# Performance work log

Hardware: AMD Instinct MI355X
Metric: run time of the kernel (lower is better)

## Reference

```python
import jax, jax.numpy as jnp
import numpy as np

H = 512  # hidden_size


def setup_inputs() -> dict:
    key = jax.random.key(0)
    ks = jax.random.split(key, 13)
    B, S, E, V = 64, 2048, 512, 32000
    s = 0.05
    return {
        "word_input": jax.random.randint(ks[0], (B,), 0, V),
        "last_hidden": jax.random.normal(ks[1], (1, B, H), jnp.float32),
        "encoder_outputs": jax.random.normal(ks[2], (S, B, H), jnp.float32),
        "emb": jax.random.normal(ks[3], (V, E), jnp.float32) * s,
        "attn_W": jax.random.normal(ks[4], (H, 2 * H), jnp.float32) * s,
        "attn_b": jax.random.normal(ks[5], (H,), jnp.float32) * s,
        "v": jax.random.normal(ks[6], (H,), jnp.float32) * s,
        "W_ih": jax.random.normal(ks[7], (3 * H, H + E), jnp.float32) * s,
        "W_hh": jax.random.normal(ks[8], (3 * H, H), jnp.float32) * s,
        "b_ih": jax.random.normal(ks[9], (3 * H,), jnp.float32) * s,
        "b_hh": jax.random.normal(ks[10], (3 * H,), jnp.float32) * s,
        "out_W": jax.random.normal(ks[11], (V, 2 * H), jnp.float32) * s,
        "out_b": jax.random.normal(ks[12], (V,), jnp.float32) * s,
    }


def reference(word_input, last_hidden, encoder_outputs, emb, attn_W, attn_b, v,
              W_ih, W_hh, b_ih, b_hh, out_W, out_b):
    # word_input: [B] int; last_hidden: [1,B,H]; encoder_outputs: [S,B,H]
    hid = last_hidden[-1]                       # [B,H]
    enc = jnp.transpose(encoder_outputs, (1, 0, 2))  # [B,S,H]

    # Bahdanau 'concat' attention: tanh(W [h;e] + b) . v  (split W to avoid [B,S,2H])
    Wa, We = attn_W[:, :H], attn_W[:, H:]
    energy = jnp.tanh((hid @ Wa.T)[:, None, :] + jnp.einsum('bsh,kh->bsk', enc, We) + attn_b)
    scores = jnp.einsum('bsk,k->bs', energy, v)       # [B,S]
    attn = jax.nn.softmax(scores, axis=1)             # [B,S]
    context = jnp.einsum('bs,bsh->bh', attn, enc)     # [B,H]

    # GRU step (PyTorch gate layout: r, z, n)
    x = jnp.concatenate([emb[word_input], context], axis=1)  # [B,E+H]
    gi = x @ W_ih.T + b_ih
    gh = hid @ W_hh.T + b_hh
    r = jax.nn.sigmoid(gi[:, :H] + gh[:, :H])
    z = jax.nn.sigmoid(gi[:, H:2 * H] + gh[:, H:2 * H])
    n = jnp.tanh(gi[:, 2 * H:] + r * gh[:, 2 * H:])
    h_new = (1.0 - z) * n + z * hid                   # [B,H]

    logits = jnp.concatenate([h_new, context], axis=1) @ out_W.T + out_b
    output = jax.nn.log_softmax(logits, axis=1)       # [B,V]
    return output, h_new[None]                        # hidden: [1,B,H]
```

## Files before the change

kernel.cpp:

```cpp
#include <hip/hip_runtime.h>
#include <hip/hip_bf16.h>
#include <cstdint>
#include <cstddef>

#define HD 512
#define BB 64
#define SS 2048
#define VV 32000
#define MM (SS*BB)
#define NCH 32

typedef __attribute__((ext_vector_type(8))) short bf16x8;
typedef __attribute__((ext_vector_type(4))) float f32x4;

static __device__ __forceinline__ unsigned pack2(float a, float b) {
    unsigned r;
    asm("v_cvt_pk_bf16_f32 %0, %1, %2" : "=v"(r) : "v"(a), "v"(b));
    return r;
}
static __device__ __forceinline__ float rcp_fast(float x) {
    float r; asm("v_rcp_f32 %0, %1" : "=v"(r) : "v"(x)); return r;
}
static __device__ __forceinline__ float tanh_fast(float x) {
    float e = __expf(2.f * x);
    return 1.f - 2.f * rcp_fast(e + 1.f);
}
static __device__ __forceinline__ float sigmoid_fast(float x) {
    return 1.f / (1.f + __expf(-x));
}
static __device__ __forceinline__ void gload16(const void* g, void* l) {
    __builtin_amdgcn_global_load_lds(
        (const __attribute__((address_space(1))) void*)g,
        (__attribute__((address_space(3))) void*)l, 16, 0, 0);
}

#define WAITL   asm volatile("s_waitcnt lgkmcnt(0)" ::: "memory")
#define WAITVL(N) asm volatile("s_waitcnt vmcnt(" #N ") lgkmcnt(0)" ::: "memory")
#define SBAR    __builtin_amdgcn_s_barrier()
#define SCHED   __builtin_amdgcn_sched_barrier(0)

__global__ void prep_kernel(const float* __restrict__ hid,
                            const float* __restrict__ attn_W,
                            const float* __restrict__ attn_b,
                            float* __restrict__ qc,
                            uint4* __restrict__ WeB4) {
    int i = blockIdx.x * 256 + threadIdx.x;
    int n = i >> 6, b = i & 63;
    const float* hrow = hid + b * HD;
    const float* wrow = attn_W + (size_t)n * (2 * HD);
    float acc = 0.f;
    for (int k = 0; k < HD; k += 4) {
        float4 h4 = *(const float4*)(hrow + k);
        float4 w4 = *(const float4*)(wrow + k);
        acc += h4.x * w4.x + h4.y * w4.y + h4.z * w4.z + h4.w * w4.w;
    }
    qc[b * HD + n] = acc + attn_b[n];
    int col = (i << 3) & 511;
    int cc0 = col >> 3;
    const float* src = attn_W + (size_t)n * (2 * HD) + HD + col;
    float4 f0 = *(const float4*)(src);
    float4 f1 = *(const float4*)(src + 4);
    uint4 p;
    p.x = pack2(f0.x, f0.y); p.y = pack2(f0.z, f0.w);
    p.z = pack2(f1.x, f1.y); p.w = pack2(f1.z, f1.w);
    WeB4[n * 64 + cc0] = p;
}

__global__ __launch_bounds__(512, 4) void fattn_kernel(
    const float* __restrict__ enc,
    const uint4* __restrict__ WeB4,
    const float* __restrict__ qc,
    const float* __restrict__ vvec,
    float* __restrict__ oP,
    float* __restrict__ lP)
{
    __shared__ uint4 Ald[64 * 8];
    __shared__ float red[64][8];
    __shared__ float p_lds[64];
    __shared__ float opart[8 * 512];

    const int tid = threadIdx.x;
    const int wv = tid >> 6, lane = tid & 63, l15 = lane & 15, l4 = lane >> 4;
    const int b = blockIdx.x & 63;
    const int c = blockIdx.x >> 6;
    const int s0 = c * 64;

    f32x4 acc[4][4] = {};

    const int arow = tid >> 3;
    const int ac8 = tid & 7;
    const float* aptr = enc + ((size_t)(s0 + arow) * 64 + b) * HD + ac8 * 8;
    const int aslot = arow * 8 + (ac8 ^ (arow & 7));

    const uint4* bbase = WeB4 + (size_t)(wv * 64 + l15) * 64 + l4;

    float4 pa[2][2];
    pa[0][0] = *(const float4*)(aptr);
    pa[0][1] = *(const float4*)(aptr + 4);

#pragma unroll
    for (int t = 0; t < 8; ++t) {
        const int cur = t & 1;
        if (t > 0) { WAITL; SBAR; SCHED; }
        {
            uint4 u;
            u.x = pack2(pa[cur][0].x, pa[cur][0].y);
            u.y = pack2(pa[cur][0].z, pa[cur][0].w);
            u.z = pack2(pa[cur][1].x, pa[cur][1].y);
            u.w = pack2(pa[cur][1].z, pa[cur][1].w);
            Ald[aslot] = u;
        }
        if (t < 7) {
            pa[cur ^ 1][0] = *(const float4*)(aptr + (t + 1) * 64);
            pa[cur ^ 1][1] = *(const float4*)(aptr + (t + 1) * 64 + 4);
        }
        WAITL; SBAR; SCHED;

#pragma unroll
        for (int ks = 0; ks < 2; ++ks) {
            const int chunk = ks * 4 + l4;
            bf16x8 af[4], bfr[4];
#pragma unroll
            for (int mi = 0; mi < 4; ++mi) {
                int row = mi * 16 + l15;
                af[mi] = *(const bf16x8*)&Ald[row * 8 + (chunk ^ (row & 7))];
            }
#pragma unroll
            for (int ni = 0; ni < 4; ++ni)
                bfr[ni] = *(const bf16x8*)(bbase + ni * 16 * 64 + t * 8 + ks * 4);
#pragma unroll
            for (int mi = 0; mi < 4; ++mi)
#pragma unroll
                for (int ni = 0; ni < 4; ++ni)
                    acc[mi][ni] = __builtin_amdgcn_mfma_f32_16x16x32_bf16(
                        af[mi], bfr[ni], acc[mi][ni], 0, 0, 0);
        }
    }

    float vv[4], qn[4];
#pragma unroll
    for (int ni = 0; ni < 4; ++ni) {
        int n = wv * 64 + ni * 16 + l15;
        vv[ni] = vvec[n];
        qn[ni] = qc[b * HD + n];
    }
#pragma unroll
    for (int mi = 0; mi < 4; ++mi) {
#pragma unroll
        for (int r = 0; r < 4; ++r) {
            const int rowl = mi * 16 + l4 * 4 + r;
            float s = 0.f;
#pragma unroll
            for (int ni = 0; ni < 4; ++ni)
                s += tanh_fast(acc[mi][ni][r] + qn[ni]) * vv[ni];
#pragma unroll
            for (int msk = 8; msk >= 1; msk >>= 1)
                s += __shfl_xor(s, msk);
            if (l15 == 0) red[rowl][wv] = s;
        }
    }
    __syncthreads();
    if (tid < 64) {
        float t = ((red[tid][0] + red[tid][1]) + (red[tid][2] + red[tid][3]))
                + ((red[tid][4] + red[tid][5]) + (red[tid][6] + red[tid][7]));
        float p = __expf(t);
        p_lds[tid] = p;
        float l = p;
#pragma unroll
        for (int msk = 32; msk >= 1; msk >>= 1) l += __shfl_xor(l, msk);
        if (tid == 0) lP[b * NCH + c] = l;
    }
    __syncthreads();

    float o8[8] = {};
    const float* ebase = enc + ((size_t)(s0 + wv * 8) * 64 + b) * HD + lane * 8;
#pragma unroll
    for (int i = 0; i < 8; ++i) {
        float w = p_lds[wv * 8 + i];
        const float* ep = ebase + (size_t)i * 64 * HD;
        float4 e0 = *(const float4*)(ep);
        float4 e1 = *(const float4*)(ep + 4);
        o8[0] += w * e0.x; o8[1] += w * e0.y; o8[2] += w * e0.z; o8[3] += w * e0.w;
        o8[4] += w * e1.x; o8[5] += w * e1.y; o8[6] += w * e1.z; o8[7] += w * e1.w;
    }
    {
        float4* dst = (float4*)&opart[wv * 512 + lane * 8];
        float4 w0 = {o8[0], o8[1], o8[2], o8[3]};
        float4 w1 = {o8[4], o8[5], o8[6], o8[7]};
        dst[0] = w0; dst[1] = w1;
    }
    __syncthreads();
    float o = 0.f;
#pragma unroll
    for (int w = 0; w < 8; ++w) o += opart[w * 512 + tid];
    oP[((size_t)b * NCH + c) * HD + tid] = o;
}

__global__ void combine_kernel(const float* __restrict__ oP,
                               const float* __restrict__ lP,
                               const int* __restrict__ word,
                               const float* __restrict__ emb,
                               float* __restrict__ x,
                               unsigned* __restrict__ y_bf) {
    const int b = blockIdx.x;
    const int tid = threadIdx.x;
    __shared__ float ctx_lds[512];
    float L = 0.f;
#pragma unroll 8
    for (int c = 0; c < NCH; ++c) L += lP[b * NCH + c];
    float o = 0.f;
#pragma unroll 4
    for (int c = 0; c < NCH; ++c)
        o += oP[((size_t)b * NCH + c) * HD + tid];
    float ctx = o / L;
    x[b * 1024 + HD + tid] = ctx;
    ctx_lds[tid] = ctx;
    x[b * 1024 + tid] = emb[(size_t)word[b] * HD + tid];
    __syncthreads();
    if (tid < 256)
        y_bf[b * 512 + 256 + tid] = pack2(ctx_lds[2 * tid], ctx_lds[2 * tid + 1]);
}

__global__ void gates_kernel(const float* __restrict__ x,
                             const float* __restrict__ hid,
                             const float* __restrict__ W_ih,
                             const float* __restrict__ W_hh,
                             const float* __restrict__ b_ih,
                             const float* __restrict__ b_hh,
                             float* __restrict__ gi, float* __restrict__ gh) {
    const int tid = threadIdx.x;
    const int b = tid & 63;
    const int j = blockIdx.x * 4 + (tid >> 6);
    float agi = 0.f, agh = 0.f;
    const float* xr = x + b * 1024;
    const float* wr = W_ih + (size_t)j * 1024;
    for (int k = 0; k < 1024; k += 4) {
        float4 xv = *(const float4*)(xr + k);
        float4 w4 = *(const float4*)(wr + k);
        agi += xv.x * w4.x + xv.y * w4.y + xv.z * w4.z + xv.w * w4.w;
    }
    const float* hr = hid + b * HD;
    const float* wh = W_hh + (size_t)j * HD;
    for (int k = 0; k < HD; k += 4) {
        float4 hv = *(const float4*)(hr + k);
        float4 w4 = *(const float4*)(wh + k);
        agh += hv.x * w4.x + hv.y * w4.y + hv.z * w4.z + hv.w * w4.w;
    }
    gi[b * 1536 + j] = agi + b_ih[j];
    gh[b * 1536 + j] = agh + b_hh[j];
}

__global__ void hnew_kernel(const float* __restrict__ gi,
                            const float* __restrict__ gh,
                            const float* __restrict__ hid,
                            float* __restrict__ out_h,
                            unsigned* __restrict__ y_bf) {
    const int b = blockIdx.x;
    const int h = threadIdx.x * 2;
    float hn[2];
#pragma unroll
    for (int j = 0; j < 2; ++j) {
        int hh = h + j;
        float r = sigmoid_fast(gi[b * 1536 + hh] + gh[b * 1536 + hh]);
        float z = sigmoid_fast(gi[b * 1536 + 512 + hh] + gh[b * 1536 + 512 + hh]);
        float n = tanh_fast(gi[b * 1536 + 1024 + hh] + r * gh[b * 1536 + 1024 + hh]);
        hn[j] = (1.f - z) * n + z * hid[b * HD + hh];
        out_h[b * HD + hh] = hn[j];
    }
    y_bf[b * 512 + (h >> 1)] = pack2(hn[0], hn[1]);
}

__global__ __launch_bounds__(256, 4) void logits_kernel(
    const unsigned short* __restrict__ y_bf,
    const float* __restrict__ out_W,
    const float* __restrict__ out_b,
    float* __restrict__ logits)
{
    __shared__ uint4 Yld[64 * 8];
    __shared__ uint4 Wld[64 * 8];
    const int tid = threadIdx.x;
    const int wv = tid >> 6, lane = tid & 63, l15 = lane & 15, l4 = lane >> 4;
    const int n0 = blockIdx.x * 64;

    f32x4 acc[4] = {};

    const int s1 = tid, s2 = tid + 256;
    const int r1 = s1 >> 3, g1 = (s1 & 7) ^ (r1 & 7);
    const int r2 = s2 >> 3, g2 = (s2 & 7) ^ (r2 & 7);
    const unsigned short* ya1 = y_bf + (size_t)r1 * 1024 + g1 * 8;
    const unsigned short* ya2 = y_bf + (size_t)r2 * 1024 + g2 * 8;

    const int wr = tid >> 3, wc8 = tid & 7;
    const int wsl = wc8 ^ (wr & 7);
    const float* wp0 = out_W + (size_t)(n0 + wr) * 1024 + wc8 * 8;
    const float* wp1 = out_W + (size_t)(n0 + wr + 32) * 1024 + wc8 * 8;

    float4 pw[2][4];
    pw[0][0] = *(const float4*)(wp0);
    pw[0][1] = *(const float4*)(wp0 + 4);
    pw[0][2] = *(const float4*)(wp1);
    pw[0][3] = *(const float4*)(wp1 + 4);

#pragma unroll
    for (int t = 0; t < 16; ++t) {
        const int cur = t & 1;
        if (t > 0) {
            WAITL; SBAR; SCHED;
        }
        gload16(ya1 + t * 64, &Yld[s1]);
        gload16(ya2 + t * 64, &Yld[s2]);
        {
            uint4 u;
            u.x = pack2(pw[cur][0].x, pw[cur][0].y);
            u.y = pack2(pw[cur][0].z, pw[cur][0].w);
            u.z = pack2(pw[cur][1].x, pw[cur][1].y);
            u.w = pack2(pw[cur][1].z, pw[cur][1].w);
            Wld[wr * 8 + wsl] = u;
            u.x = pack2(pw[cur][2].x, pw[cur][2].y);
            u.y = pack2(pw[cur][2].z, pw[cur][2].w);
            u.z = pack2(pw[cur][3].x, pw[cur][3].y);
            u.w = pack2(pw[cur][3].z, pw[cur][3].w);
            Wld[(wr + 32) * 8 + wsl] = u;
        }
        if (t < 15) {
            const int k1 = (t + 1) * 64;
            pw[cur ^ 1][0] = *(const float4*)(wp0 + k1);
            pw[cur ^ 1][1] = *(const float4*)(wp0 + k1 + 4);
            pw[cur ^ 1][2] = *(const float4*)(wp1 + k1);
            pw[cur ^ 1][3] = *(const float4*)(wp1 + k1 + 4);
            WAITVL(4);
        } else {
            WAITVL(0);
        }
        SBAR; SCHED;

#pragma unroll
        for (int ks = 0; ks < 2; ++ks) {
            const int chunk = ks * 4 + l4;
            bf16x8 af[4], bfr;
#pragma unroll
            for (int mi = 0; mi < 4; ++mi) {
                int row = mi * 16 + l15;
                af[mi] = *(const bf16x8*)&Yld[row * 8 + (chunk ^ (row & 7))];
            }
            {
                int row = wv * 16 + l15;
                bfr = *(const bf16x8*)&Wld[row * 8 + (chunk ^ (row & 7))];
            }
#pragma unroll
            for (int mi = 0; mi < 4; ++mi)
                acc[mi] = __builtin_amdgcn_mfma_f32_16x16x32_bf16(
                    af[mi], bfr, acc[mi], 0, 0, 0);
        }
    }
#pragma unroll
    for (int mi = 0; mi < 4; ++mi) {
#pragma unroll
        for (int r = 0; r < 4; ++r) {
            const int b = mi * 16 + l4 * 4 + r;
            int n = n0 + wv * 16 + l15;
            logits[(size_t)b * VV + n] = acc[mi][r] + out_b[n];
        }
    }
}

__global__ void lsm1_kernel(const float* __restrict__ logits,
                            float* __restrict__ part) {
    const int bid = blockIdx.x;
    const int b = bid / 5, q = bid - b * 5;
    const int tid = threadIdx.x;
    __shared__ float sm[256];
    const float* row = logits + (size_t)b * VV + q * 6400;
    float m = -1e30f;
    for (int i = tid; i < 6400; i += 256) m = fmaxf(m, row[i]);
    sm[tid] = m; __syncthreads();
    for (int o = 128; o > 0; o >>= 1) {
        if (tid < o) sm[tid] = fmaxf(sm[tid], sm[tid + o]);
        __syncthreads();
    }
    m = sm[0]; __syncthreads();
    float s = 0.f;
    for (int i = tid; i < 6400; i += 256) s += __expf(row[i] - m);
    sm[tid] = s; __syncthreads();
    for (int o = 128; o > 0; o >>= 1) {
        if (tid < o) sm[tid] += sm[tid + o];
        __syncthreads();
    }
    if (tid == 0) { part[bid * 2] = m; part[bid * 2 + 1] = sm[0]; }
}

__global__ void lsm2_kernel(float* __restrict__ logits,
                            const float* __restrict__ part) {
    const int bid = blockIdx.x;
    const int b = bid / 5, q = bid - b * 5;
    const int tid = threadIdx.x;
    float m = -1e30f;
#pragma unroll
    for (int c = 0; c < 5; ++c) m = fmaxf(m, part[(b * 5 + c) * 2]);
    float L = 0.f;
#pragma unroll
    for (int c = 0; c < 5; ++c)
        L += part[(b * 5 + c) * 2 + 1] * __expf(part[(b * 5 + c) * 2] - m);
    float lse = m + __logf(L);
    float* row = logits + (size_t)b * VV + q * 6400;
    for (int i = tid; i < 6400; i += 256) row[i] -= lse;
}

extern "C" void kernel_launch(void* const* d_in, const int* in_sizes, int n_in,
                              void* d_out, int out_size, void* d_ws, size_t ws_size,
                              hipStream_t stream) {
    (void)in_sizes; (void)n_in; (void)out_size; (void)ws_size;
    const int*   word   = (const int*)d_in[0];
    const float* hid    = (const float*)d_in[1];
    const float* enc    = (const float*)d_in[2];
    const float* emb    = (const float*)d_in[3];
    const float* attn_W = (const float*)d_in[4];
    const float* attn_b = (const float*)d_in[5];
    const float* v      = (const float*)d_in[6];
    const float* W_ih   = (const float*)d_in[7];
    const float* W_hh   = (const float*)d_in[8];
    const float* b_ih   = (const float*)d_in[9];
    const float* b_hh   = (const float*)d_in[10];
    const float* out_W  = (const float*)d_in[11];
    const float* out_b  = (const float*)d_in[12];

    float* out    = (float*)d_out;
    float* logits = out;
    float* out_h  = out + (size_t)BB * VV;

    char* ws0 = (char*)d_ws;
    size_t off = 0;
    float* qc      = (float*)(ws0 + off);    off += 64 * 512 * 4;
    uint4* WeB4    = (uint4*)(ws0 + off);    off += 512 * 512 * 2;
    float* oP      = (float*)(ws0 + off);    off += (size_t)BB * NCH * HD * 4;
    float* lP      = (float*)(ws0 + off);    off += BB * NCH * 4;
    float* x       = (float*)(ws0 + off);    off += 64 * 1024 * 4;
    unsigned* y_bf = (unsigned*)(ws0 + off); off += 64 * 1024 * 2;
    float* gi      = (float*)(ws0 + off);    off += 64 * 1536 * 4;
    float* gh      = (float*)(ws0 + off);    off += 64 * 1536 * 4;
    float* lsmp    = (float*)(ws0 + off);    off += 320 * 2 * 4;

    prep_kernel<<<128, 256, 0, stream>>>(hid, attn_W, attn_b, qc, WeB4);
    fattn_kernel<<<BB * NCH, 512, 0, stream>>>(enc, WeB4, qc, v, oP, lP);
    combine_kernel<<<BB, 512, 0, stream>>>(oP, lP, word, emb, x, y_bf);
    gates_kernel<<<384, 256, 0, stream>>>(x, hid, W_ih, W_hh, b_ih, b_hh, gi, gh);
    hnew_kernel<<<BB, 256, 0, stream>>>(gi, gh, hid, out_h, y_bf);
    logits_kernel<<<VV / 64, 256, 0, stream>>>((const unsigned short*)y_bf, out_W, out_b, logits);
    lsm1_kernel<<<320, 256, 0, stream>>>(logits, lsmp);
    lsm2_kernel<<<320, 256, 0, stream>>>(logits, lsmp);
}
```

Before: 373.0 us.

## Stage full encoder tile in LDS upfront and pre-swizzle We into fragment order

The attention kernel now loads and converts the whole 64x512 encoder tile into a 64KB LDS buffer in one pass with a single barrier, replacing the per-k-step double-buffered register pipeline with its two barriers per step. The prep kernel writes the bf16 We matrix in MFMA-fragment order so each lane's B loads are contiguous and coalesced. opart aliases the same LDS. The larger LDS footprint (~66KB per 512-thread block) may lower occupancy below the launch-bounds target of 4 blocks, and global loads no longer overlap with MFMA work.

New measurement: 321.6 us. 13.8% less time.

```diff
diff --git a/kernel.cpp b/kernel.cpp
--- a/kernel.cpp
+++ b/kernel.cpp
@@ -43,9 +43,11 @@
                             const float* __restrict__ attn_W,
                             const float* __restrict__ attn_b,
                             float* __restrict__ qc,
-                            uint4* __restrict__ WeB4) {
+                            uint4* __restrict__ WeF) {
     int i = blockIdx.x * 256 + threadIdx.x;
-    int n = i >> 6, b = i & 63;
+    int n = i >> 6;
+    int cc = i & 63;
+    int b = i & 63;
     const float* hrow = hid + b * HD;
     const float* wrow = attn_W + (size_t)n * (2 * HD);
     float acc = 0.f;
@@ -55,29 +57,31 @@
         acc += h4.x * w4.x + h4.y * w4.y + h4.z * w4.z + h4.w * w4.w;
     }
     qc[b * HD + n] = acc + attn_b[n];
-    int col = (i << 3) & 511;
-    int cc0 = col >> 3;
-    const float* src = attn_W + (size_t)n * (2 * HD) + HD + col;
+    const float* src = attn_W + (size_t)n * (2 * HD) + HD + cc * 8;
     float4 f0 = *(const float4*)(src);
     float4 f1 = *(const float4*)(src + 4);
     uint4 p;
     p.x = pack2(f0.x, f0.y); p.y = pack2(f0.z, f0.w);
     p.z = pack2(f1.x, f1.y); p.w = pack2(f1.z, f1.w);
-    WeB4[n * 64 + cc0] = p;
+    int wv = n >> 6, ni = (n >> 4) & 3, l15 = n & 15;
+    int t = cc >> 3, ks = (cc >> 2) & 1, l4 = cc & 3;
+    int lane = l4 * 16 + l15;
+    WeF[((((wv * 8 + t) * 2 + ks) * 4 + ni) << 6) + lane] = p;
 }
 
 __global__ __launch_bounds__(512, 4) void fattn_kernel(
     const float* __restrict__ enc,
-    const uint4* __restrict__ WeB4,
+    const uint4* __restrict__ WeF,
     const float* __restrict__ qc,
     const float* __restrict__ vvec,
     float* __restrict__ oP,
     float* __restrict__ lP)
 {
-    __shared__ uint4 Ald[64 * 8];
-    __shared__ float red[64][8];
-    __shared__ float p_lds[64];
-    __shared__ float opart[8 * 512];
+    __shared__ char smem[65536 + 2048 + 256];
+    uint4* Ald = (uint4*)smem;
+    float (*red)[8] = (float(*)[8])(smem + 65536);
+    float* p_lds = (float*)(smem + 65536 + 2048);
+    float* opart = (float*)smem;
 
     const int tid = threadIdx.x;
     const int wv = tid >> 6, lane = tid & 63, l15 = lane & 15, l4 = lane >> 4;
@@ -85,49 +89,39 @@
     const int c = blockIdx.x >> 6;
     const int s0 = c * 64;
 
+    {
+        const int arow = tid >> 3, a8 = tid & 7;
+        const float* ap = enc + ((size_t)(s0 + arow) * 64 + b) * HD;
+#pragma unroll
+        for (int j = 0; j < 8; ++j) {
+            int cc = j * 8 + a8;
+            float4 f0 = *(const float4*)(ap + cc * 8);
+            float4 f1 = *(const float4*)(ap + cc * 8 + 4);
+            uint4 u;
+            u.x = pack2(f0.x, f0.y); u.y = pack2(f0.z, f0.w);
+            u.z = pack2(f1.x, f1.y); u.w = pack2(f1.z, f1.w);
+            Ald[arow * 64 + j * 8 + (a8 ^ (arow & 7))] = u;
+        }
+    }
+    __syncthreads();
+
     f32x4 acc[4][4] = {};
-
-    const int arow = tid >> 3;
-    const int ac8 = tid & 7;
-    const float* aptr = enc + ((size_t)(s0 + arow) * 64 + b) * HD + ac8 * 8;
-    const int aslot = arow * 8 + (ac8 ^ (arow & 7));
-
-    const uint4* bbase = WeB4 + (size_t)(wv * 64 + l15) * 64 + l4;
-
-    float4 pa[2][2];
-    pa[0][0] = *(const float4*)(aptr);
-    pa[0][1] = *(const float4*)(aptr + 4);
+    const uint4* bbase = WeF + wv * 4096 + lane;
 
 #pragma unroll
     for (int t = 0; t < 8; ++t) {
-        const int cur = t & 1;
-        if (t > 0) { WAITL; SBAR; SCHED; }
-        {
-            uint4 u;
-            u.x = pack2(pa[cur][0].x, pa[cur][0].y);
-            u.y = pack2(pa[cur][0].z, pa[cur][0].w);
-            u.z = pack2(pa[cur][1].x, pa[cur][1].y);
-            u.w = pack2(pa[cur][1].z, pa[cur][1].w);
-            Ald[aslot] = u;
-        }
-        if (t < 7) {
-            pa[cur ^ 1][0] = *(const float4*)(aptr + (t + 1) * 64);
-            pa[cur ^ 1][1] = *(const float4*)(aptr + (t + 1) * 64 + 4);
-        }
-        WAITL; SBAR; SCHED;
-
 #pragma unroll
         for (int ks = 0; ks < 2; ++ks) {
-            const int chunk = ks * 4 + l4;
             bf16x8 af[4], bfr[4];
 #pragma unroll
             for (int mi = 0; mi < 4; ++mi) {
                 int row = mi * 16 + l15;
-                af[mi] = *(const bf16x8*)&Ald[row * 8 + (chunk ^ (row & 7))];
+                af[mi] = *(const bf16x8*)&Ald[row * 64 + t * 8
+                                              + ((ks * 4 + l4) ^ (row & 7))];
             }
 #pragma unroll
             for (int ni = 0; ni < 4; ++ni)
-                bfr[ni] = *(const bf16x8*)(bbase + ni * 16 * 64 + t * 8 + ks * 4);
+                bfr[ni] = *(const bf16x8*)(bbase + t * 512 + ks * 256 + ni * 64);
 #pragma unroll
             for (int mi = 0; mi < 4; ++mi)
 #pragma unroll
@@ -431,7 +425,7 @@
     char* ws0 = (char*)d_ws;
     size_t off = 0;
     float* qc      = (float*)(ws0 + off);    off += 64 * 512 * 4;
-    uint4* WeB4    = (uint4*)(ws0 + off);    off += 512 * 512 * 2;
+    uint4* WeF     = (uint4*)(ws0 + off);    off += 512 * 512 * 2;
     float* oP      = (float*)(ws0 + off);    off += (size_t)BB * NCH * HD * 4;
     float* lP      = (float*)(ws0 + off);    off += BB * NCH * 4;
     float* x       = (float*)(ws0 + off);    off += 64 * 1024 * 4;
@@ -440,8 +434,8 @@
     float* gh      = (float*)(ws0 + off);    off += 64 * 1536 * 4;
     float* lsmp    = (float*)(ws0 + off);    off += 320 * 2 * 4;
 
-    prep_kernel<<<128, 256, 0, stream>>>(hid, attn_W, attn_b, qc, WeB4);
-    fattn_kernel<<<BB * NCH, 512, 0, stream>>>(enc, WeB4, qc, v, oP, lP);
+    prep_kernel<<<128, 256, 0, stream>>>(hid, attn_W, attn_b, qc, WeF);
+    fattn_kernel<<<BB * NCH, 512, 0, stream>>>(enc, WeF, qc, v, oP, lP);
     combine_kernel<<<BB, 512, 0, stream>>>(oP, lP, word, emb, x, y_bf);
     gates_kernel<<<384, 256, 0, stream>>>(x, hid, W_ih, W_hh, b_ih, b_hh, gi, gh);
     hnew_kernel<<<BB, 256, 0, stream>>>(gi, gh, hid, out_h, y_bf);
```

## Stage swizzled bf16 We tiles through LDS instead of direct global fragment loads

Applied to the files above, without the earlier changes.

The attention-weight matrix is now stored with an XOR swizzle, and each k-step it is loaded cooperatively into a 64KB LDS buffer with direct global-to-LDS loads, replacing per-wave strided global fragment reads. The register double-buffered A-tile prefetch is dropped in favour of a simple sync/load/sync loop, and MFMA sections get raised wave priority. LDS use grows sharply, so launch bounds drop to 2 blocks per CU, trading occupancy and prefetch overlap for coalesced, conflict-free B-operand access.

Result: faster. 340.9 us (-8.6%).

```diff
diff --git a/kernel.cpp b/kernel.cpp
--- a/kernel.cpp
+++ b/kernel.cpp
@@ -63,10 +63,11 @@
     uint4 p;
     p.x = pack2(f0.x, f0.y); p.y = pack2(f0.z, f0.w);
     p.z = pack2(f1.x, f1.y); p.w = pack2(f1.z, f1.w);
-    WeB4[n * 64 + cc0] = p;
-}
-
-__global__ __launch_bounds__(512, 4) void fattn_kernel(
+    int ccs = (cc0 & ~7) | ((cc0 & 7) ^ (n & 7));
+    WeB4[n * 64 + ccs] = p;
+}
+
+__global__ __launch_bounds__(512, 2) void fattn_kernel(
     const float* __restrict__ enc,
     const uint4* __restrict__ WeB4,
     const float* __restrict__ qc,
@@ -74,10 +75,12 @@
     float* __restrict__ oP,
     float* __restrict__ lP)
 {
-    __shared__ uint4 Ald[64 * 8];
-    __shared__ float red[64][8];
-    __shared__ float p_lds[64];
-    __shared__ float opart[8 * 512];
+    __shared__ char smem[8192 + 65536 + 2048 + 256];
+    uint4* Ald = (uint4*)smem;
+    uint4* Bld = (uint4*)(smem + 8192);
+    float (*red)[8] = (float(*)[8])(smem + 8192 + 65536);
+    float* p_lds = (float*)(smem + 8192 + 65536 + 2048);
+    float* opart = (float*)(smem + 8192);
 
     const int tid = threadIdx.x;
     const int wv = tid >> 6, lane = tid & 63, l15 = lane & 15, l4 = lane >> 4;
@@ -92,30 +95,23 @@
     const float* aptr = enc + ((size_t)(s0 + arow) * 64 + b) * HD + ac8 * 8;
     const int aslot = arow * 8 + (ac8 ^ (arow & 7));
 
-    const uint4* bbase = WeB4 + (size_t)(wv * 64 + l15) * 64 + l4;
-
-    float4 pa[2][2];
-    pa[0][0] = *(const float4*)(aptr);
-    pa[0][1] = *(const float4*)(aptr + 4);
-
-#pragma unroll
+    const int brow = wv * 8 + (lane >> 3);
+    const uint4* bg = WeB4 + (size_t)brow * 64 + (lane & 7);
+
     for (int t = 0; t < 8; ++t) {
-        const int cur = t & 1;
-        if (t > 0) { WAITL; SBAR; SCHED; }
-        {
-            uint4 u;
-            u.x = pack2(pa[cur][0].x, pa[cur][0].y);
-            u.y = pack2(pa[cur][0].z, pa[cur][0].w);
-            u.z = pack2(pa[cur][1].x, pa[cur][1].y);
-            u.w = pack2(pa[cur][1].z, pa[cur][1].w);
-            Ald[aslot] = u;
-        }
-        if (t < 7) {
-            pa[cur ^ 1][0] = *(const float4*)(aptr + (t + 1) * 64);
-            pa[cur ^ 1][1] = *(const float4*)(aptr + (t + 1) * 64 + 4);
-        }
-        WAITL; SBAR; SCHED;
-
+        __syncthreads();
+        float4 a0 = *(const float4*)(aptr + t * 64);
+        float4 a1 = *(const float4*)(aptr + t * 64 + 4);
+#pragma unroll
+        for (int i = 0; i < 8; ++i)
+            gload16(bg + (size_t)i * 64 * 64 + t * 8, &Bld[i * 512 + tid]);
+        uint4 u;
+        u.x = pack2(a0.x, a0.y); u.y = pack2(a0.z, a0.w);
+        u.z = pack2(a1.x, a1.y); u.w = pack2(a1.z, a1.w);
+        Ald[aslot] = u;
+        __syncthreads();
+
+        __builtin_amdgcn_s_setprio(1);
 #pragma unroll
         for (int ks = 0; ks < 2; ++ks) {
             const int chunk = ks * 4 + l4;
@@ -126,8 +122,10 @@
                 af[mi] = *(const bf16x8*)&Ald[row * 8 + (chunk ^ (row & 7))];
             }
 #pragma unroll
-            for (int ni = 0; ni < 4; ++ni)
-                bfr[ni] = *(const bf16x8*)(bbase + ni * 16 * 64 + t * 8 + ks * 4);
+            for (int ni = 0; ni < 4; ++ni) {
+                int row = wv * 64 + ni * 16 + l15;
+                bfr[ni] = *(const bf16x8*)&Bld[row * 8 + (chunk ^ (row & 7))];
+            }
 #pragma unroll
             for (int mi = 0; mi < 4; ++mi)
 #pragma unroll
@@ -135,6 +133,7 @@
                     acc[mi][ni] = __builtin_amdgcn_mfma_f32_16x16x32_bf16(
                         af[mi], bfr[ni], acc[mi][ni], 0, 0, 0);
         }
+        __builtin_amdgcn_s_setprio(0);
     }
 
     float vv[4], qn[4];
```
